# Performance work log

Hardware: AMD Instinct MI355X
Metric: run time of the kernel (lower is better)

Reference implementation:

```python
import jax, jax.numpy as jnp
import numpy as np

DIM = 128
WS = 16      # window size
HALO = 8     # halo size
HEADS = 8
HD = DIM // HEADS
HIDDEN = DIM * 4
EPS = 1e-5


def _ln(x, w, b):
    # LayerNorm over last (channel) axis, like nn.LayerNorm(channels)
    mu = jnp.mean(x, axis=-1, keepdims=True)
    var = jnp.var(x, axis=-1, keepdims=True)
    return (x - mu) * jax.lax.rsqrt(var + EPS) * w + b


def _halo_windows(t):
    # t: [B,H,W,C] -> overlapping halo windows [B,nH,nW,K*K,C]
    B, H, W, C = t.shape
    K = WS + 2 * HALO
    nH, nW = H // WS, W // WS
    tp = jnp.pad(t, ((0, 0), (HALO, HALO), (HALO, HALO), (0, 0)))
    ih = jnp.arange(nH)[:, None] * WS + jnp.arange(K)[None, :]  # [nH,K]
    iw = jnp.arange(nW)[:, None] * WS + jnp.arange(K)[None, :]  # [nW,K]
    t1 = tp[:, ih]            # [B,nH,K,W+2h,C]
    t2 = t1[:, :, :, iw]      # [B,nH,K,nW,K,C]
    return t2.transpose(0, 1, 3, 2, 4, 5).reshape(B, nH, nW, K * K, C)


def _query_windows(t):
    # t: [B,H,W,C] -> non-overlapping windows [B,nH,nW,WS*WS,C]
    B, H, W, C = t.shape
    nH, nW = H // WS, W // WS
    return (t.reshape(B, nH, WS, nW, WS, C)
             .transpose(0, 1, 3, 2, 4, 5)
             .reshape(B, nH, nW, WS * WS, C))


def _halo_attention(h, qkv_w, qkv_b, proj_w, proj_b):
    # h: [B,H,W,C] channels-last
    B, H, W, C = h.shape
    nH, nW = H // WS, W // WS
    K = WS + 2 * HALO
    qkv = h @ qkv_w.T + qkv_b                       # [B,H,W,3C]
    q, k, v = jnp.split(qkv, 3, axis=-1)
    qw = _query_windows(q).reshape(B, nH, nW, WS * WS, HEADS, HD)
    kw = _halo_windows(k).reshape(B, nH, nW, K * K, HEADS, HD)
    vw = _halo_windows(v).reshape(B, nH, nW, K * K, HEADS, HD)
    scale = HD ** -0.5
    scores = jnp.einsum('bxyqhd,bxykhd->bxyhqk', qw * scale, kw)
    attn = jax.nn.softmax(scores, axis=-1)
    out = jnp.einsum('bxyhqk,bxykhd->bxyqhd', attn, vw)
    out = (out.reshape(B, nH, nW, WS, WS, C)
              .transpose(0, 1, 3, 2, 4, 5)
              .reshape(B, H, W, C))
    return out @ proj_w.T + proj_b


def setup_inputs() -> dict:
    key = jax.random.key(0)
    ks = jax.random.split(key, 12)
    s = lambda k, shape, fan: jax.random.normal(k, shape, jnp.float32) * (fan ** -0.5)
    return {
        'x': jax.random.normal(ks[0], (1, DIM, 128, 128), jnp.float32),
        'ln1_w': jnp.ones((DIM,), jnp.float32),
        'ln1_b': jnp.zeros((DIM,), jnp.float32),
        'qkv_w': s(ks[1], (3 * DIM, DIM), DIM),
        'qkv_b': jnp.zeros((3 * DIM,), jnp.float32),
        'proj_w': s(ks[2], (DIM, DIM), DIM),
        'proj_b': jnp.zeros((DIM,), jnp.float32),
        'ln2_w': jnp.ones((DIM,), jnp.float32),
        'ln2_b': jnp.zeros((DIM,), jnp.float32),
        'fc1_w': s(ks[3], (HIDDEN, DIM), DIM),
        'fc1_b': jnp.zeros((HIDDEN,), jnp.float32),
        'fc2_w': s(ks[4], (DIM, HIDDEN), HIDDEN),
        'fc2_b': jnp.zeros((DIM,), jnp.float32),
    }


def reference(x, ln1_w, ln1_b, qkv_w, qkv_b, proj_w, proj_b,
              ln2_w, ln2_b, fc1_w, fc1_b, fc2_w, fc2_b):
    # x: [B,C,H,W]
    xh = x.transpose(0, 2, 3, 1)                    # BHWC
    h = _ln(xh, ln1_w, ln1_b)
    attn_out = _halo_attention(h, qkv_w, qkv_b, proj_w, proj_b)
    xh = xh + attn_out                              # residual 1
    h2 = _ln(xh, ln2_w, ln2_b)
    m = jax.nn.gelu(h2 @ fc1_w.T + fc1_b, approximate=False) @ fc2_w.T + fc2_b
    xh = xh + m                                     # residual 2 (dropout=0)
    return xh.transpose(0, 3, 1, 2)                 # back to NCHW
```

## Files before the change

### kernel.cpp

```cpp
#include <hip/hip_runtime.h>
#include <hip/hip_bf16.h>


typedef __attribute__((ext_vector_type(8))) short bf16x8;
typedef __attribute__((ext_vector_type(4))) float f32x4;
typedef __attribute__((ext_vector_type(4))) unsigned int u32x4;

#define MFMA16(a, b, c) __builtin_amdgcn_mfma_f32_16x16x32_bf16((a), (b), (c), 0, 0, 0)

__device__ __forceinline__ float u2f(unsigned short u) {
  unsigned int x = ((unsigned int)u) << 16;
  return __builtin_bit_cast(float, x);
}
__device__ __forceinline__ unsigned short f2u(float f) {
  unsigned int x = __builtin_bit_cast(unsigned int, f);
  x += 0x7FFFu + ((x >> 16) & 1u);
  return (unsigned short)(x >> 16);
}
__device__ __forceinline__ unsigned int cvt_pk_bf16(float lo, float hi) {
  unsigned int r;
  asm("v_cvt_pk_bf16_f32 %0, %1, %2" : "=v"(r) : "v"(lo), "v"(hi));
  return r;
}
__device__ __forceinline__ float gelu_f(float v) {
  const float y = 0.7978845608f * (v + 0.044715f * v * v * v);
  const float E = __builtin_amdgcn_exp2f(y * 2.8853900818f);
  return v - v * __builtin_amdgcn_rcpf(E + 1.0f);
}

#define QSCALE 0.36067376022224085f

#define O_XHT 0ull
#define O_H1  (8ull << 20)
#define O_QB  (12ull << 20)
#define O_XH1 (16ull << 20)
#define O_KP  (24ull << 20)
#define O_VPT (O_KP + 5308416ull)
#define O_WB  (O_KP + (16ull << 20))
#define PADT  20736

__global__ __launch_bounds__(256) void setup_kernel(
    const float* __restrict__ a, const float* __restrict__ b,
    const float* __restrict__ c, const float* __restrict__ d,
    unsigned short* __restrict__ wb,
    unsigned short* __restrict__ kp, unsigned short* __restrict__ vpt) {
  const int bx = blockIdx.x, tid = threadIdx.x;
  if (bx < 192) {
    const int i = (bx * 256 + tid) * 4;
    const float* s; int lo;
    if (i < 49152)       { s = a; lo = 0; }
    else if (i < 65536)  { s = b; lo = 49152; }
    else if (i < 131072) { s = c; lo = 65536; }
    else                 { s = d; lo = 131072; }
    const float4 v = *(const float4*)(s + (i - lo));
    ushort4 o;
    o.x = f2u(v.x); o.y = f2u(v.y); o.z = f2u(v.z); o.w = f2u(v.w);
    *(ushort4*)(wb + i) = o;
  } else if (bx < 209) {
    const int idx = (bx - 192) * 256 + tid;
    if (idx >= 4352) return;
    int r, cc;
    if (idx < 2304) {
      const int rr = idx / 144;
      r = (rr < 8) ? rr : rr + 128;
      cc = idx - rr * 144;
    } else {
      const int i2 = idx - 2304;
      r = 8 + (i2 >> 4);
      const int c2 = i2 & 15;
      cc = (c2 < 8) ? c2 : c2 + 128;
    }
    const size_t off = ((size_t)r * 144 + cc) * 128;
    const u32x4 z = {};
#pragma unroll
    for (int k = 0; k < 16; k++) *(u32x4*)(kp + off + k * 8) = z;
  } else {
    const int ch = bx - 209;
    unsigned short* base = vpt + (size_t)ch * PADT;
    const u32x4 z = {};
    if (tid < 144) {
      *(u32x4*)(base + tid * 8) = z;
      *(u32x4*)(base + 19584 + tid * 8) = z;
    }
    const int hr = tid >> 1, side = tid & 1;
    *(u32x4*)(base + (hr + 8) * 144 + side * 136) = z;
  }
}

__global__ __launch_bounds__(256) void ln1_kernel(
    const float* __restrict__ x,
    const float* __restrict__ lw, const float* __restrict__ lb,
    float* __restrict__ xh_t, unsigned short* __restrict__ h1) {
  __shared__ float ld[128][33];
  const int t0 = blockIdx.x * 32;
  const int tid = threadIdx.x;
  {
    const int c = tid >> 1, th = (tid & 1) * 16;
    const float* src = x + (size_t)c * 16384 + t0 + th;
#pragma unroll
    for (int i = 0; i < 4; i++) {
      const float4 v = *(const float4*)(src + i * 4);
      ld[c][th + i * 4]     = v.x;
      ld[c][th + i * 4 + 1] = v.y;
      ld[c][th + i * 4 + 2] = v.z;
      ld[c][th + i * 4 + 3] = v.w;
    }
  }
  __syncthreads();
  const int t = tid >> 3, cp = (tid & 7) * 16;
  float vals[16];
  float s = 0.f, q = 0.f;
#pragma unroll
  for (int i = 0; i < 16; i++) {
    const float v = ld[cp + i][t];
    vals[i] = v;
    s += v; q += v * v;
  }
  s += __shfl_xor(s, 1); q += __shfl_xor(q, 1);
  s += __shfl_xor(s, 2); q += __shfl_xor(q, 2);
  s += __shfl_xor(s, 4); q += __shfl_xor(q, 4);
  const float mu = s * 0.0078125f;
  const float rs = rsqrtf(q * 0.0078125f - mu * mu + 1e-5f);
  float* xrow = xh_t + (size_t)(t0 + t) * 128 + cp;
#pragma unroll
  for (int i = 0; i < 4; i++)
    *(float4*)(xrow + i * 4) =
        float4{vals[4*i], vals[4*i+1], vals[4*i+2], vals[4*i+3]};
  unsigned int pk[8];
#pragma unroll
  for (int k = 0; k < 8; k++) {
    const float y0 = (vals[2*k]   - mu) * rs * lw[cp + 2*k]   + lb[cp + 2*k];
    const float y1 = (vals[2*k+1] - mu) * rs * lw[cp + 2*k+1] + lb[cp + 2*k+1];
    pk[k] = cvt_pk_bf16(y0, y1);
  }
  unsigned int* hrow = (unsigned int*)(h1 + (size_t)(t0 + t) * 128 + cp);
  *(u32x4*)(hrow)     = u32x4{pk[0], pk[1], pk[2], pk[3]};
  *(u32x4*)(hrow + 4) = u32x4{pk[4], pk[5], pk[6], pk[7]};
}

__global__ __launch_bounds__(64) void qkv_kernel(
    const unsigned short* __restrict__ A,
    const unsigned short* __restrict__ B,
    const float* __restrict__ bias,
    unsigned short* __restrict__ qb,
    unsigned short* __restrict__ kp,
    unsigned short* __restrict__ vpt) {
  const int tid = threadIdx.x;
  const int lr = tid & 15, lg = tid >> 4;
  const int mB = blockIdx.x * 64, nB = blockIdx.y * 64;
  f32x4 acc[4][4] = {};
  const unsigned short* Ab = A + (size_t)(mB + lr) * 128 + lg * 8;
  const unsigned short* Bb = B + (size_t)(nB + lr) * 128 + lg * 8;
  for (int k = 0; k < 128; k += 32) {
    bf16x8 a[4], b[4];
#pragma unroll
    for (int i = 0; i < 4; i++) {
      a[i] = *(const bf16x8*)(Ab + (size_t)i * 16 * 128 + k);
      b[i] = *(const bf16x8*)(Bb + (size_t)i * 16 * 128 + k);
    }
#pragma unroll
    for (int i = 0; i < 4; i++)
#pragma unroll
      for (int j = 0; j < 4; j++)
        acc[i][j] = MFMA16(a[i], b[j], acc[i][j]);
  }

  if (nB < 256) {
#pragma unroll
    for (int j = 0; j < 4; j++) {
      const int jj = nB + j * 16 + lr;
      const float bv = bias[jj];
#pragma unroll
      for (int i = 0; i < 4; i++)
#pragma unroll
        for (int r = 0; r < 4; r++) {
          const int ii = mB + i * 16 + lg * 4 + r;
          const float v = acc[i][j][r] + bv;
          if (jj < 128) {
            qb[(size_t)ii * 128 + jj] = f2u(v * QSCALE);
          } else {
            const int gh = ii >> 7, gw = ii & 127;
            const size_t prow = (size_t)(gh + 8) * 144 + (gw + 8);
            kp[prow * 128 + (jj - 128)] = f2u(v);
          }
        }
    }
  } else {
    __shared__ __align__(16) unsigned short tbv[64][72];
#pragma unroll
    for (int j = 0; j < 4; j++) {
      const int jl = j * 16 + lr;
      const float bv = bias[nB + jl];
#pragma unroll
      for (int i = 0; i < 4; i++)
#pragma unroll
        for (int r = 0; r < 4; r++) {
          const int il = i * 16 + lg * 4 + r;
          tbv[jl][il] = f2u(acc[i][j][r] + bv);
        }
    }
    __syncthreads();
    const int gh = mB >> 7, gw0 = mB & 127;
    const size_t prow0 = (size_t)(gh + 8) * 144 + gw0 + 8;
    unsigned short* dst = vpt + (size_t)(nB - 256 + tid) * PADT + prow0;
#pragma unroll
    for (int t8 = 0; t8 < 8; t8++)
      *(u32x4*)(dst + t8 * 8) = *(const u32x4*)&tbv[tid][t8 * 8];
  }
}

__global__ __launch_bounds__(256) void projln2_kernel(
    const unsigned short* __restrict__ A,
    const unsigned short* __restrict__ B,
    const float* __restrict__ bias,
    const float* __restrict__ xh_t,
    const float* __restrict__ lw, const float* __restrict__ lb,
    float* __restrict__ xh1, unsigned short* __restrict__ h2) {
  __shared__ float sred[4][16][2];
  const int tid = threadIdx.x;
  const int w = tid >> 6, l = tid & 63;
  const int lr = l & 15, lg = l >> 4;
  const int mB = blockIdx.x * 16;
  const int n0 = w * 32;
  f32x4 acc[2] = {};
  const unsigned short* Ar = A + (size_t)(mB + lr) * 128 + lg * 8;
  const unsigned short* Br0 = B + (size_t)(n0 + lr) * 128 + lg * 8;
  const unsigned short* Br1 = Br0 + 16 * 128;
  for (int k = 0; k < 128; k += 32) {
    const bf16x8 a  = *(const bf16x8*)(Ar + k);
    const bf16x8 b0 = *(const bf16x8*)(Br0 + k);
    const bf16x8 b1 = *(const bf16x8*)(Br1 + k);
    acc[0] = MFMA16(a, b0, acc[0]);
    acc[1] = MFMA16(a, b1, acc[1]);
  }
  float vv[2][4];
#pragma unroll
  for (int j = 0; j < 2; j++) {
    const int jj = n0 + j * 16 + lr;
    const float bv = bias[jj];
#pragma unroll
    for (int r = 0; r < 4; r++) {
      const int ii = mB + lg * 4 + r;
      const float v = acc[j][r] + bv + xh_t[(size_t)ii * 128 + jj];
      xh1[(size_t)ii * 128 + jj] = v;
      vv[j][r] = v;
    }
  }
#pragma unroll
  for (int r = 0; r < 4; r++) {
    float s = vv[0][r] + vv[1][r];
    float q = vv[0][r] * vv[0][r] + vv[1][r] * vv[1][r];
    s += __shfl_xor(s, 1); q += __shfl_xor(q, 1);
    s += __shfl_xor(s, 2); q += __shfl_xor(q, 2);
    s += __shfl_xor(s, 4); q += __shfl_xor(q, 4);
    s += __shfl_xor(s, 8); q += __shfl_xor(q, 8);
    if (lr == 0) {
      sred[w][lg * 4 + r][0] = s;
      sred[w][lg * 4 + r][1] = q;
    }
  }
  __syncthreads();
#pragma unroll
  for (int r = 0; r < 4; r++) {
    const int tok = lg * 4 + r;
    const float s = sred[0][tok][0] + sred[1][tok][0] +
                    sred[2][tok][0] + sred[3][tok][0];
    const float q = sred[0][tok][1] + sred[1][tok][1] +
                    sred[2][tok][1] + sred[3][tok][1];
    const float mu = s * 0.0078125f;
    const float rs = rsqrtf(q * 0.0078125f - mu * mu + 1e-5f);
#pragma unroll
    for (int j = 0; j < 2; j++) {
      const int jj = n0 + j * 16 + lr;
      const float y = (vv[j][r] - mu) * rs * lw[jj] + lb[jj];
      h2[(size_t)(mB + tok) * 128 + jj] = f2u(y);
    }
  }
}

__global__ __launch_bounds__(256) void mlp_kernel(
    const unsigned short* __restrict__ h2,
    const unsigned short* __restrict__ fc1_wb,
    const float* __restrict__ fc1_b,
    const unsigned short* __restrict__ fc2_wb,
    const float* __restrict__ fc2_b,
    const float* __restrict__ xh1,
    float* __restrict__ outp) {
  __shared__ __align__(16) char smem[66560];
  unsigned short (*m_lds)[520] = (unsigned short(*)[520])smem;
  float (*tb)[68] = (float(*)[68])smem;

  const int tid = threadIdx.x;
  const int w = tid >> 6, l = tid & 63;
  const int lr = l & 15, lg = l >> 4;
  const int mB = blockIdx.x * 64;

  {
    f32x4 acc[8][4] = {};
    const unsigned short* Ab = fc1_wb + (size_t)(w * 128 + lr) * 128 + lg * 8;
    const unsigned short* Bb = h2 + (size_t)(mB + lr) * 128 + lg * 8;
    for (int k = 0; k < 128; k += 32) {
      bf16x8 a[8], b[4];
#pragma unroll
      for (int i = 0; i < 8; i++)
        a[i] = *(const bf16x8*)(Ab + (size_t)i * 16 * 128 + k);
#pragma unroll
      for (int j = 0; j < 4; j++)
        b[j] = *(const bf16x8*)(Bb + (size_t)j * 16 * 128 + k);
#pragma unroll
      for (int i = 0; i < 8; i++)
#pragma unroll
        for (int j = 0; j < 4; j++)
          acc[i][j] = MFMA16(a[i], b[j], acc[i][j]);
    }
#pragma unroll
    for (int i = 0; i < 8; i++) {
      const int n0 = w * 128 + i * 16 + lg * 4;
      const float4 b4 = *(const float4*)(fc1_b + n0);
#pragma unroll
      for (int j = 0; j < 4; j++) {
        const int t = j * 16 + lr;
        const float g0 = gelu_f(acc[i][j][0] + b4.x);
        const float g1 = gelu_f(acc[i][j][1] + b4.y);
        const float g2 = gelu_f(acc[i][j][2] + b4.z);
        const float g3 = gelu_f(acc[i][j][3] + b4.w);
        uint2 pk;
        pk.x = cvt_pk_bf16(g0, g1);
        pk.y = cvt_pk_bf16(g2, g3);
        *(uint2*)&m_lds[t][n0] = pk;
      }
    }
  }
  __syncthreads();

  f32x4 acc2[4][2] = {};
  {
    const unsigned short* Bb = fc2_wb + (size_t)(w * 32 + lr) * 512 + lg * 8;
    for (int k = 0; k < 512; k += 32) {
      bf16x8 a[4], b[2];
#pragma unroll
      for (int i = 0; i < 4; i++)
        a[i] = *(const bf16x8*)&m_lds[i * 16 + lr][k + lg * 8];
#pragma unroll
      for (int j = 0; j < 2; j++)
        b[j] = *(const bf16x8*)(Bb + (size_t)j * 16 * 512 + k);
#pragma unroll
      for (int i = 0; i < 4; i++)
#pragma unroll
        for (int j = 0; j < 2; j++)
          acc2[i][j] = MFMA16(a[i], b[j], acc2[i][j]);
    }
  }
  __syncthreads();

#pragma unroll
  for (int j = 0; j < 2; j++) {
    const int jj = w * 32 + j * 16 + lr;
    const float bv = fc2_b[jj];
#pragma unroll
    for (int i = 0; i < 4; i++)
#pragma unroll
      for (int r = 0; r < 4; r++) {
        const int il = i * 16 + lg * 4 + r;
        tb[jj][il] = acc2[i][j][r] + bv +
                     xh1[(size_t)(mB + il) * 128 + jj];
      }
  }
  __syncthreads();
  {
    const int c = tid >> 1, seg = (tid & 1) * 32;
    float* op = outp + (size_t)c * 16384 + mB + seg;
#pragma unroll
    for (int q = 0; q < 8; q++)
      *(float4*)(op + q * 4) = *(const float4*)&tb[c][seg + q * 4];
  }
}

__global__ __launch_bounds__(256) void attn_kernel(
    const unsigned short* __restrict__ qb,
    const unsigned short* __restrict__ kp,
    const unsigned short* __restrict__ vpt,
    unsigned short* __restrict__ attnb) {
  __shared__ __align__(16) unsigned int pl[4][16][20];
  __shared__ __align__(16) unsigned short K_lds[32][32][16];
  const int bid = blockIdx.x;
  const int win = bid & 63;
  const int sub = bid >> 6;
  const int qh = sub & 1, head = sub >> 1;
  const int wy = win >> 3, wx = win & 7;
  const int tid = threadIdx.x;
  const int wv = tid >> 6, l = tid & 63;
  const int lr = l & 15, lg = l >> 4;

#pragma unroll
  for (int it = 0; it < 4; it++) {
    const int idx = it * 256 + tid;
    const int krr = idx >> 5, key = idx & 31;
    const unsigned short* src =
        kp + ((size_t)(wy * 16 + krr) * 144 + wx * 16 + key) * 128 + head * 16;
    *(u32x4*)&K_lds[krr][key][0] = *(const u32x4*)src;
    *(u32x4*)&K_lds[krr][key][8] = *(const u32x4*)(src + 8);
  }

  bf16x8 qf[2];
#pragma unroll
  for (int qt = 0; qt < 2; qt++) {
    bf16x8 t = {};
    if (lg < 2) {
      const int qi = qh * 128 + wv * 32 + qt * 16 + lr;
      const int gh = wy * 16 + (qi >> 4), gw = wx * 16 + (qi & 15);
      t = *(const bf16x8*)(qb + ((size_t)(gh * 128 + gw)) * 128 + head * 16 + lg * 8);
    }
    qf[qt] = t;
  }

  bf16x8 ones;
#pragma unroll
  for (int e = 0; e < 8; e++) ones[e] = (short)0x3F80;

  f32x4 acc[2] = {}, den[2] = {};
  unsigned int* wp = &pl[wv][lr][lg * 4];
  const unsigned int* rp = &pl[wv][lr][(lg & 1) * 8];
  const unsigned int psel = (lg >= 2) ? 0x07060302u : 0x05040100u;

  const unsigned short* vbase =
      vpt + (size_t)(head * 16 + lr) * PADT + (size_t)(wy * 16) * 144 + wx * 16 + lg * 8;

  __syncthreads();

  for (int kr = 0; kr < 32; kr++) {
    bf16x8 kf0 = {}, kf1 = {};
    if (lg < 2) {
      kf0 = *(const bf16x8*)&K_lds[kr][lr][lg * 8];
      kf1 = *(const bf16x8*)&K_lds[kr][16 + lr][lg * 8];
    }
    const bf16x8 vf = *(const bf16x8*)(vbase + kr * 144);
#pragma unroll
    for (int qt = 0; qt < 2; qt++) {
      f32x4 s0 = {}, s1 = {};
      s0 = MFMA16(kf0, qf[qt], s0);
      s1 = MFMA16(kf1, qf[qt], s1);
      unsigned int pk[4];
#pragma unroll
      for (int r = 0; r < 4; r++)
        pk[r] = cvt_pk_bf16(__builtin_amdgcn_exp2f(s0[r]),
                            __builtin_amdgcn_exp2f(s1[r]));
      *(u32x4*)wp = u32x4{pk[0], pk[1], pk[2], pk[3]};
      const u32x4 in0 = *(const u32x4*)(rp);
      const u32x4 in1 = *(const u32x4*)(rp + 4);
      u32x4 pa;
      pa[0] = __builtin_amdgcn_perm(in0[1], in0[0], psel);
      pa[1] = __builtin_amdgcn_perm(in0[3], in0[2], psel);
      pa[2] = __builtin_amdgcn_perm(in1[1], in1[0], psel);
      pa[3] = __builtin_amdgcn_perm(in1[3], in1[2], psel);
      const bf16x8 paf = __builtin_bit_cast(bf16x8, pa);
      acc[qt] = MFMA16(paf, vf, acc[qt]);
      den[qt] = MFMA16(paf, ones, den[qt]);
    }
  }

#pragma unroll
  for (int qt = 0; qt < 2; qt++)
#pragma unroll
    for (int r = 0; r < 4; r++) {
      const int q0 = qt * 16 + lg * 4 + r;
      const int qi2 = qh * 128 + wv * 32 + q0;
      const int gh2 = wy * 16 + (qi2 >> 4), gw2 = wx * 16 + (qi2 & 15);
      attnb[((size_t)(gh2 * 128 + gw2)) * 128 + head * 16 + lr] =
          f2u(acc[qt][r] * __builtin_amdgcn_rcpf(den[qt][r]));
    }
}

extern "C" void kernel_launch(void* const* d_in, const int* in_sizes, int n_in,
                              void* d_out, int out_size, void* d_ws, size_t ws_size,
                              hipStream_t stream) {
  const float* x      = (const float*)d_in[0];
  const float* ln1w   = (const float*)d_in[1];
  const float* ln1b   = (const float*)d_in[2];
  const float* qkv_w  = (const float*)d_in[3];
  const float* qkv_b  = (const float*)d_in[4];
  const float* proj_w = (const float*)d_in[5];
  const float* proj_b = (const float*)d_in[6];
  const float* ln2w   = (const float*)d_in[7];
  const float* ln2b   = (const float*)d_in[8];
  const float* fc1_w  = (const float*)d_in[9];
  const float* fc1_b  = (const float*)d_in[10];
  const float* fc2_w  = (const float*)d_in[11];
  const float* fc2_b  = (const float*)d_in[12];

  char* ws = (char*)d_ws;
  float*          xh_t = (float*)(ws + O_XHT);
  unsigned short* h1   = (unsigned short*)(ws + O_H1);
  unsigned short* qb   = (unsigned short*)(ws + O_QB);
  float*          xh1  = (float*)(ws + O_XH1);
  unsigned short* kp   = (unsigned short*)(ws + O_KP);
  unsigned short* vpt  = (unsigned short*)(ws + O_VPT);
  unsigned short* wb   = (unsigned short*)(ws + O_WB);
  unsigned short* attnb = h1;
  unsigned short* h2    = qb;
  float* outp = (float*)d_out;

  unsigned short* qkv_wb  = wb;
  unsigned short* proj_wb = wb + 49152;
  unsigned short* fc1_wb  = wb + 65536;
  unsigned short* fc2_wb  = wb + 131072;

  setup_kernel<<<337, 256, 0, stream>>>(qkv_w, proj_w, fc1_w, fc2_w, wb, kp, vpt);
  ln1_kernel<<<512, 256, 0, stream>>>(x, ln1w, ln1b, xh_t, h1);
  qkv_kernel<<<dim3(256, 6), 64, 0, stream>>>(h1, qkv_wb, qkv_b, qb, kp, vpt);
  attn_kernel<<<1024, 256, 0, stream>>>(qb, kp, vpt, attnb);
  projln2_kernel<<<1024, 256, 0, stream>>>(
      attnb, proj_wb, proj_b, xh_t, ln2w, ln2b, xh1, h2);
  mlp_kernel<<<256, 256, 0, stream>>>(h2, fc1_wb, fc1_b, fc2_wb, fc2_b, xh1, outp);
}
```

Before: 96.61 us.

## Feed softmax probabilities directly as MFMA B operand, drop LDS transpose

The attention kernel no longer round-trips the exp'd score fragments through a per-wave LDS buffer with byte-permutes to transpose them. It swaps the PV MFMA operand order so the probability registers can be used directly as the B fragment. V is loaded as two 8-byte pieces and interleaved with perms to match the new key ordering. The output is then written as packed bf16 pairs using a single reciprocal of the denominator per row. This removes LDS writes/reads and a sync-free shuffle from the inner loop, but depends on the key permutation across the two MFMA halves matching the V interleave exactly.

```diff
diff --git a/kernel.cpp b/kernel.cpp
--- a/kernel.cpp
+++ b/kernel.cpp
@@ -381,7 +381,6 @@
     const unsigned short* __restrict__ kp,
     const unsigned short* __restrict__ vpt,
     unsigned short* __restrict__ attnb) {
-  __shared__ __align__(16) unsigned int pl[4][16][20];
   __shared__ __align__(16) unsigned short K_lds[32][32][16];
   const int bid = blockIdx.x;
   const int win = bid & 63;
@@ -419,12 +418,9 @@
   for (int e = 0; e < 8; e++) ones[e] = (short)0x3F80;
 
   f32x4 acc[2] = {}, den[2] = {};
-  unsigned int* wp = &pl[wv][lr][lg * 4];
-  const unsigned int* rp = &pl[wv][lr][(lg & 1) * 8];
-  const unsigned int psel = (lg >= 2) ? 0x07060302u : 0x05040100u;
-
-  const unsigned short* vbase =
-      vpt + (size_t)(head * 16 + lr) * PADT + (size_t)(wy * 16) * 144 + wx * 16 + lg * 8;
+
+  const unsigned short* vrow =
+      vpt + (size_t)(head * 16 + lr) * PADT + (size_t)(wy * 16) * 144 + wx * 16;
 
   __syncthreads();
 
@@ -434,41 +430,41 @@
       kf0 = *(const bf16x8*)&K_lds[kr][lr][lg * 8];
       kf1 = *(const bf16x8*)&K_lds[kr][16 + lr][lg * 8];
     }
-    const bf16x8 vf = *(const bf16x8*)(vbase + kr * 144);
+    const unsigned short* vr = vrow + kr * 144;
+    const uint2 ua = *(const uint2*)(vr + lg * 4);
+    const uint2 ub = *(const uint2*)(vr + 16 + lg * 4);
+    u32x4 vfw;
+    vfw[0] = __builtin_amdgcn_perm(ub.x, ua.x, 0x05040100u);
+    vfw[1] = __builtin_amdgcn_perm(ub.x, ua.x, 0x07060302u);
+    vfw[2] = __builtin_amdgcn_perm(ub.y, ua.y, 0x05040100u);
+    vfw[3] = __builtin_amdgcn_perm(ub.y, ua.y, 0x07060302u);
+    const bf16x8 vfrag = __builtin_bit_cast(bf16x8, vfw);
 #pragma unroll
     for (int qt = 0; qt < 2; qt++) {
       f32x4 s0 = {}, s1 = {};
       s0 = MFMA16(kf0, qf[qt], s0);
       s1 = MFMA16(kf1, qf[qt], s1);
-      unsigned int pk[4];
+      u32x4 pw;
 #pragma unroll
       for (int r = 0; r < 4; r++)
-        pk[r] = cvt_pk_bf16(__builtin_amdgcn_exp2f(s0[r]),
+        pw[r] = cvt_pk_bf16(__builtin_amdgcn_exp2f(s0[r]),
                             __builtin_amdgcn_exp2f(s1[r]));
-      *(u32x4*)wp = u32x4{pk[0], pk[1], pk[2], pk[3]};
-      const u32x4 in0 = *(const u32x4*)(rp);
-      const u32x4 in1 = *(const u32x4*)(rp + 4);
-      u32x4 pa;
-      pa[0] = __builtin_amdgcn_perm(in0[1], in0[0], psel);
-      pa[1] = __builtin_amdgcn_perm(in0[3], in0[2], psel);
-      pa[2] = __builtin_amdgcn_perm(in1[1], in1[0], psel);
-      pa[3] = __builtin_amdgcn_perm(in1[3], in1[2], psel);
-      const bf16x8 paf = __builtin_bit_cast(bf16x8, pa);
-      acc[qt] = MFMA16(paf, vf, acc[qt]);
-      den[qt] = MFMA16(paf, ones, den[qt]);
-    }
-  }
-
-#pragma unroll
-  for (int qt = 0; qt < 2; qt++)
-#pragma unroll
-    for (int r = 0; r < 4; r++) {
-      const int q0 = qt * 16 + lg * 4 + r;
-      const int qi2 = qh * 128 + wv * 32 + q0;
-      const int gh2 = wy * 16 + (qi2 >> 4), gw2 = wx * 16 + (qi2 & 15);
-      attnb[((size_t)(gh2 * 128 + gw2)) * 128 + head * 16 + lr] =
-          f2u(acc[qt][r] * __builtin_amdgcn_rcpf(den[qt][r]));
-    }
+      const bf16x8 pfrag = __builtin_bit_cast(bf16x8, pw);
+      acc[qt] = MFMA16(vfrag, pfrag, acc[qt]);
+      den[qt] = MFMA16(ones,  pfrag, den[qt]);
+    }
+  }
+
+#pragma unroll
+  for (int qt = 0; qt < 2; qt++) {
+    const float inv = __builtin_amdgcn_rcpf(den[qt][0]);
+    const int qi2 = qh * 128 + wv * 32 + qt * 16 + lr;
+    const int gh2 = wy * 16 + (qi2 >> 4), gw2 = wx * 16 + (qi2 & 15);
+    uint2 o;
+    o.x = cvt_pk_bf16(acc[qt][0] * inv, acc[qt][1] * inv);
+    o.y = cvt_pk_bf16(acc[qt][2] * inv, acc[qt][3] * inv);
+    *(uint2*)(attnb + ((size_t)(gh2 * 128 + gw2)) * 128 + head * 16 + lg * 4) = o;
+  }
 }
 
 extern "C" void kernel_launch(void* const* d_in, const int* in_sizes, int n_in,
```

Measured after the change: 102.7 us. +6.4%, slower.
